# Kernel tuning notes

Measured on AMD Instinct MI355X. Metric: run time of the kernel, lower is better.

Reference implementation:

```python
import jax, jax.numpy as jnp
import numpy as np

B, T, D_IN, H, N_LAYERS, D_OUT = 256, 512, 128, 512, 3, 1


def setup_inputs() -> dict:
    key = jax.random.key(0)
    ks = jax.random.split(key, 20)
    s = 1.0 / np.sqrt(H)
    inp = {"x": jax.random.normal(ks[0], (B, T, D_IN), dtype=jnp.float32)}
    k = 1
    for l in range(N_LAYERS):
        d_in = D_IN if l == 0 else H
        inp[f"W_ih_{l}"] = jax.random.uniform(ks[k], (4 * H, d_in), minval=-s, maxval=s); k += 1
        inp[f"W_hh_{l}"] = jax.random.uniform(ks[k], (4 * H, H), minval=-s, maxval=s); k += 1
        inp[f"b_ih_{l}"] = jax.random.uniform(ks[k], (4 * H,), minval=-s, maxval=s); k += 1
        inp[f"b_hh_{l}"] = jax.random.uniform(ks[k], (4 * H,), minval=-s, maxval=s); k += 1
    inp["W_fc"] = jax.random.uniform(ks[k], (D_OUT, H), minval=-s, maxval=s); k += 1
    inp["b_fc"] = jax.random.uniform(ks[k], (D_OUT,), minval=-s, maxval=s)
    return inp


def _lstm_layer(x, W_ih, W_hh, b_ih, b_hh):
    # x: [B, T, d_in] -> hs: [B, T, H]. PyTorch gate order: i, f, g, o.
    xg = jnp.einsum("btd,gd->btg", x, W_ih) + b_ih + b_hh  # precompute input proj [B,T,4H]
    Hh = W_hh.shape[1]
    Bb = x.shape[0]

    def step(carry, xg_t):
        h, c = carry
        g = xg_t + h @ W_hh.T  # [B, 4H]
        i, f, gg, o = jnp.split(g, 4, axis=-1)
        c = jax.nn.sigmoid(f) * c + jax.nn.sigmoid(i) * jnp.tanh(gg)
        h = jax.nn.sigmoid(o) * jnp.tanh(c)
        return (h, c), h

    h0 = jnp.zeros((Bb, Hh), x.dtype)
    (_, _), hs = jax.lax.scan(step, (h0, h0), jnp.swapaxes(xg, 0, 1))
    return jnp.swapaxes(hs, 0, 1)


def reference(x, W_ih_0, W_hh_0, b_ih_0, b_hh_0,
              W_ih_1, W_hh_1, b_ih_1, b_hh_1,
              W_ih_2, W_hh_2, b_ih_2, b_hh_2,
              W_fc, b_fc):
    # Eval mode: inter-layer dropout (p=0.4) is identity.
    h = _lstm_layer(x, W_ih_0, W_hh_0, b_ih_0, b_hh_0)
    h = _lstm_layer(h, W_ih_1, W_hh_1, b_ih_1, b_hh_1)
    h = _lstm_layer(h, W_ih_2, W_hh_2, b_ih_2, b_hh_2)
    return h[:, -1, :] @ W_fc.T + b_fc  # [B, D_OUT]
```

## Files before the change

### kernel.cpp

```cpp
#include <hip/hip_runtime.h>

#define B_   256
#define T_   512
#define DIN_ 128
#define H_   512
#define G4_  2048

typedef __bf16 bf16_t;
typedef __bf16 bf16x8 __attribute__((ext_vector_type(8)));
typedef __bf16 bf16x4 __attribute__((ext_vector_type(4)));
typedef float  f32x4  __attribute__((ext_vector_type(4)));

__device__ __forceinline__ void gload16cc(const void* g, void* l) {
  __builtin_amdgcn_global_load_lds(
      (const __attribute__((address_space(1))) unsigned int*)g,
      (__attribute__((address_space(3))) unsigned int*)l, 16, 0, 17);
}

__global__ void cast_f32_bf16(const float* __restrict__ s, bf16_t* __restrict__ d, int n) {
  int i = (blockIdx.x * 256 + threadIdx.x) * 4;
  if (i >= n) return;
  float4 v = *(const float4*)(s + i);
  bf16x4 o;
  o[0] = (bf16_t)v.x; o[1] = (bf16_t)v.y; o[2] = (bf16_t)v.z; o[3] = (bf16_t)v.w;
  *(bf16x4*)(d + i) = o;
}

__global__ void cast_strided(const float* __restrict__ s, bf16_t* __restrict__ d,
                             int Ks, int Kd, int coff) {
  int npr = Ks >> 3;
  int i = blockIdx.x * 256 + threadIdx.x;
  if (i >= 2048 * npr) return;
  int row = i / npr, j = i - row * npr;
  const float* sp = s + (size_t)row * Ks + j * 8;
  float4 v0 = *(const float4*)sp;
  float4 v1 = *(const float4*)(sp + 4);
  bf16x8 o;
  o[0] = (bf16_t)v0.x; o[1] = (bf16_t)v0.y; o[2] = (bf16_t)v0.z; o[3] = (bf16_t)v0.w;
  o[4] = (bf16_t)v1.x; o[5] = (bf16_t)v1.y; o[6] = (bf16_t)v1.z; o[7] = (bf16_t)v1.w;
  *(bf16x8*)(d + (size_t)row * Kd + coff + j * 8) = o;
}

__global__ void bias_sum(const float* __restrict__ a, const float* __restrict__ b,
                         float* __restrict__ o, int n) {
  int i = blockIdx.x * 256 + threadIdx.x;
  if (i < n) o[i] = a[i] + b[i];
}

#define RING_N (8 * 256 * 512)
#define FSTR   16

template<int NKT>
__device__ __forceinline__ void step_loop(
    char* smem, const bf16_t* __restrict__ xbf, const bf16_t* __restrict__ wcl,
    const float* __restrict__ bias_l, bf16_t* ringPrev, bf16_t* ringOwn,
    float* __restrict__ hsf, int* flags, int layer, int bg, int ug)
{
  constexpr int KL   = NKT * 32;
  constexpr int ROWB = KL * 2;
  constexpr int XKT  = NKT - 16;
  constexpr bool L0  = (NKT == 20);
  const int tid  = threadIdx.x;
  const int lane = tid & 63;
  const int wv   = tid >> 6;
  const int ul   = lane & 15;
  const int grp  = lane >> 4;
  const int u0   = ug * 32;
  const int gsel = wv >> 1;
  const int usub = (wv & 1) * 16;

  bf16x8 wfrag[NKT];
  {
    const bf16_t* wrow = wcl + (size_t)(gsel * 512 + u0 + usub + ul) * KL + grp * 8;
    #pragma unroll
    for (int kk = 0; kk < NKT; ++kk) wfrag[kk] = *(const bf16x8*)(wrow + kk * 32);
  }
  const int um = tid >> 3;
  const int uq = tid & 7;
  float bsv[4][4];
  #pragma unroll
  for (int g = 0; g < 4; ++g)
    #pragma unroll
    for (int q = 0; q < 4; ++q)
      bsv[g][q] = bias_l[g * 512 + u0 + uq * 4 + q];

  float cst[4] = {0.f, 0.f, 0.f, 0.f};
  float* gatesF = (float*)smem;

  int* fl_own  = flags + ((layer * 512) * 4 + bg) * FSTR;
  int* fl_prev = flags + (((layer - 1) * 512) * 4 + bg) * FSTR;
  int* fl_next = flags + (((layer + 1) * 512) * 4 + bg) * FSTR;

  for (int s = 0; s < 512; ++s) {
    const int slot  = s & 7;
    const int slot2 = (s - 1) & 7;
    if (!L0) {
      if (tid == 0)
        while (__hip_atomic_load(fl_prev + s * 4 * FSTR, __ATOMIC_RELAXED,
                                 __HIP_MEMORY_SCOPE_AGENT) < 16)
          __builtin_amdgcn_s_sleep(1);
      __syncthreads();
      const bf16_t* prvS = ringPrev + (size_t)slot * (256 * 512) + (size_t)(bg * 64) * 512;
      #pragma unroll
      for (int i = 0; i < 8; ++i) {
        int r = i * 8 + wv;
        gload16cc(prvS + r * 512 + (lane ^ (r & 7)) * 8, smem + r * 2048);
      }
    } else {
      #pragma unroll
      for (int i2 = 0; i2 < 2; ++i2) {
        int idx = i2 * 512 + tid;
        int r = idx >> 4, cx = idx & 15;
        int px = cx ^ (r & 7);
        bf16x8 v = *(const bf16x8*)(xbf + ((size_t)(bg * 64 + r) * T_ + s) * 128 + cx * 8);
        *(bf16x8*)(smem + r * 1280 + px * 16) = v;
      }
    }
    __syncthreads();
    f32x4 acc[4] = {};
    #pragma unroll
    for (int kk = 0; kk < XKT; ++kk) {
      bf16x8 av[4];
      #pragma unroll
      for (int mt = 0; mt < 4; ++mt) {
        int r = mt * 16 + ul;
        int c = kk * 4 + grp;
        av[mt] = *(const bf16x8*)(smem + r * ROWB + (c ^ (r & 7)) * 16);
      }
      #pragma unroll
      for (int mt = 0; mt < 4; ++mt)
        acc[mt] = __builtin_amdgcn_mfma_f32_16x16x32_bf16(av[mt], wfrag[kk], acc[mt], 0, 0, 0);
    }
    if (tid == 0) {
      if (s > 0)
        while (__hip_atomic_load(fl_own + (s - 1) * 4 * FSTR, __ATOMIC_RELAXED,
                                 __HIP_MEMORY_SCOPE_AGENT) < 16)
          __builtin_amdgcn_s_sleep(1);
      if (layer < 2 && s >= 8)
        while (__hip_atomic_load(fl_next + (s - 8) * 4 * FSTR, __ATOMIC_RELAXED,
                                 __HIP_MEMORY_SCOPE_AGENT) < 16)
          __builtin_amdgcn_s_sleep(1);
    }
    __syncthreads();
    {
      const bf16_t* ownS = ringOwn + (size_t)slot2 * (256 * 512) + (size_t)(bg * 64) * 512;
      #pragma unroll
      for (int i = 0; i < 8; ++i) {
        int r = i * 8 + wv;
        const bf16_t* src = ownS + r * 512 + (lane ^ (r & 7)) * 8;
        if (L0) gload16cc(src, smem + r * 1280 + 256);
        else    gload16cc(src, smem + r * 2048 + 1024);
      }
    }
    __syncthreads();
    #pragma unroll
    for (int kk = XKT; kk < NKT; ++kk) {
      bf16x8 av[4];
      #pragma unroll
      for (int mt = 0; mt < 4; ++mt) {
        int r = mt * 16 + ul;
        int c = kk * 4 + grp;
        int pos;
        if (L0) pos = 16 + ((c - 16) ^ (r & 7));
        else    pos = c ^ (r & 7);
        av[mt] = *(const bf16x8*)(smem + r * ROWB + pos * 16);
      }
      #pragma unroll
      for (int mt = 0; mt < 4; ++mt)
        acc[mt] = __builtin_amdgcn_mfma_f32_16x16x32_bf16(av[mt], wfrag[kk], acc[mt], 0, 0, 0);
    }
    __syncthreads();
    #pragma unroll
    for (int mt = 0; mt < 4; ++mt)
      #pragma unroll
      for (int rr = 0; rr < 4; ++rr) {
        int m = mt * 16 + grp * 4 + rr;
        gatesF[m * 148 + gsel * 36 + usub + ul] = acc[mt][rr];
      }
    __syncthreads();
    f32x4 gi = *(const f32x4*)&gatesF[um * 148 +   0 + uq * 4];
    f32x4 gf = *(const f32x4*)&gatesF[um * 148 +  36 + uq * 4];
    f32x4 gg = *(const f32x4*)&gatesF[um * 148 +  72 + uq * 4];
    f32x4 go = *(const f32x4*)&gatesF[um * 148 + 108 + uq * 4];
    union { bf16x4 v; unsigned long long u; } pk;
    f32x4 hvf;
    #pragma unroll
    for (int q = 0; q < 4; ++q) {
      float i_ = gi[q] + bsv[0][q];
      float f_ = gf[q] + bsv[1][q];
      float g_ = gg[q] + bsv[2][q];
      float o_ = go[q] + bsv[3][q];
      float si = 1.f / (1.f + __expf(-i_));
      float sf = 1.f / (1.f + __expf(-f_));
      float so = 1.f / (1.f + __expf(-o_));
      float tg = 2.f / (1.f + __expf(-2.f * g_)) - 1.f;
      float cv = sf * cst[q] + si * tg;
      cst[q] = cv;
      float th = 2.f / (1.f + __expf(-2.f * cv)) - 1.f;
      hvf[q] = so * th;
      pk.v[q] = (bf16_t)hvf[q];
    }
    {
      int b = bg * 64 + um;
      bf16_t* dst = ringOwn + (size_t)slot * (256 * 512) + (size_t)b * 512 + u0 + uq * 4;
      (void)__hip_atomic_exchange((unsigned long long*)dst, pk.u,
                                  __ATOMIC_RELAXED, __HIP_MEMORY_SCOPE_AGENT);
      if (layer == 2 && s == 511)
        *(f32x4*)(hsf + (size_t)b * 512 + u0 + uq * 4) = hvf;
    }
    __syncthreads();
    if (tid == 0)
      atomicAdd(fl_own + s * 4 * FSTR, 1);
  }
}

__global__ __launch_bounds__(512, 2)
void lstm_persist(const bf16_t* __restrict__ xbf, const bf16_t* __restrict__ wc,
                  const float* __restrict__ bias, bf16_t* __restrict__ rings,
                  float* __restrict__ hsf, int* __restrict__ flags)
{
  __shared__ __align__(16) char smem[131072];
  const int bid   = blockIdx.x;
  const int layer = bid >> 6;
  const int bg    = (bid >> 4) & 3;
  const int ug    = bid & 15;
  bf16_t* ringOwn  = rings + (size_t)layer * RING_N;
  bf16_t* ringPrev = rings + (size_t)(layer - 1) * RING_N;
  if (layer == 0) {
    step_loop<20>(smem, xbf, wc, bias, ringPrev, ringOwn, hsf, flags, 0, bg, ug);
  } else {
    const bf16_t* wcl = wc + 2048 * 640 + (size_t)(layer - 1) * 2048 * 1024;
    step_loop<32>(smem, xbf, wcl, bias + layer * 2048, ringPrev, ringOwn, hsf,
                  flags, layer, bg, ug);
  }
}

__global__ void fc_kernel(const float* __restrict__ h, const float* __restrict__ Wfc,
                          const float* __restrict__ bfc, float* __restrict__ out) {
  int b = blockIdx.x;
  int l = threadIdx.x;
  const float* hp = h + (size_t)b * H_;
  float acc = 0.f;
  #pragma unroll
  for (int i = 0; i < 8; ++i) acc += hp[l + i * 64] * Wfc[l + i * 64];
  #pragma unroll
  for (int off = 32; off; off >>= 1) acc += __shfl_down(acc, off, 64);
  if (l == 0) out[b] = acc + bfc[0];
}

extern "C" void kernel_launch(void* const* d_in, const int* in_sizes, int n_in,
                              void* d_out, int out_size, void* d_ws, size_t ws_size,
                              hipStream_t stream) {
  const float* x        = (const float*)d_in[0];
  const float* Wih_f[3] = {(const float*)d_in[1], (const float*)d_in[5], (const float*)d_in[9]};
  const float* Whh_f[3] = {(const float*)d_in[2], (const float*)d_in[6], (const float*)d_in[10]};
  const float* bih_f[3] = {(const float*)d_in[3], (const float*)d_in[7], (const float*)d_in[11]};
  const float* bhh_f[3] = {(const float*)d_in[4], (const float*)d_in[8], (const float*)d_in[12]};
  const float* Wfc = (const float*)d_in[13];
  const float* bfc = (const float*)d_in[14];

  char* ws = (char*)d_ws;
  size_t off = 0;
  auto take = [&](size_t bytes) { char* p = ws + off; off = (off + bytes + 255) & ~255ULL; return p; };
  bf16_t* XBF   = (bf16_t*)take((size_t)B_ * T_ * DIN_ * 2);
  bf16_t* WC    = (bf16_t*)take((size_t)(2048*640 + 2*2048*1024) * 2);
  float*  BIAS  = (float*) take(3 * 2048 * 4);
  bf16_t* RINGS = (bf16_t*)take((size_t)3 * RING_N * 2);
  float*  HSF   = (float*) take((size_t)B_ * H_ * 4);
  int*    FLAGS = (int*)   take(3 * 512 * 4 * FSTR * 4);

  bf16_t* WC1 = WC + 2048 * 640;
  bf16_t* WC2 = WC1 + 2048 * 1024;

  cast_f32_bf16<<<16384, 256, 0, stream>>>(x, XBF, B_ * T_ * DIN_);
  cast_strided<<<128, 256, 0, stream>>>(Wih_f[0], WC,  128, 640, 0);
  cast_strided<<<512, 256, 0, stream>>>(Whh_f[0], WC,  512, 640, 128);
  cast_strided<<<512, 256, 0, stream>>>(Wih_f[1], WC1, 512, 1024, 0);
  cast_strided<<<512, 256, 0, stream>>>(Whh_f[1], WC1, 512, 1024, 512);
  cast_strided<<<512, 256, 0, stream>>>(Wih_f[2], WC2, 512, 1024, 0);
  cast_strided<<<512, 256, 0, stream>>>(Whh_f[2], WC2, 512, 1024, 512);
  for (int l = 0; l < 3; ++l)
    bias_sum<<<8, 256, 0, stream>>>(bih_f[l], bhh_f[l], BIAS + l * 2048, G4_);
  hipMemsetAsync(RINGS, 0, (size_t)3 * RING_N * 2, stream);
  hipMemsetAsync(FLAGS, 0, 3 * 512 * 4 * FSTR * 4, stream);

  lstm_persist<<<192, 512, 0, stream>>>(XBF, WC, BIAS, RINGS, HSF, FLAGS);
  fc_kernel<<<B_, 64, 0, stream>>>(HSF, Wfc, bfc, (float*)d_out);
}
```

Baseline: 3.853 ms.

## Switch recurrent step to 32x32x16 MFMA with split-K across wave halves

Replaces the 16x16x32 MFMA tiling with 32x32x16 MFMAs. Each wave now owns one gate's 32 units over 64 batch rows, and the K dimension is split between two wave groups whose partial sums are reduced through shared memory before the gate nonlinearities. The LDS swizzle is widened to 16 chunks and rows are stored at a uniform ROWB stride. The intent is fewer LDS A-fragment reads per MFMA and better matrix-core efficiency on the latency-bound per-timestep GEMM. The cost is an extra partial-sum reduction in LDS, a larger gate scratch buffer, and more accumulator registers.

```diff
diff --git a/kernel.cpp b/kernel.cpp
--- a/kernel.cpp
+++ b/kernel.cpp
@@ -10,6 +10,7 @@
 typedef __bf16 bf16x8 __attribute__((ext_vector_type(8)));
 typedef __bf16 bf16x4 __attribute__((ext_vector_type(4)));
 typedef float  f32x4  __attribute__((ext_vector_type(4)));
+typedef float  f32x16 __attribute__((ext_vector_type(16)));
 
 __device__ __forceinline__ void gload16cc(const void* g, void* l) {
   __builtin_amdgcn_global_load_lds(
@@ -50,42 +51,48 @@
 #define RING_N (8 * 256 * 512)
 #define FSTR   16
 
-template<int NKT>
+template<bool L0>
 __device__ __forceinline__ void step_loop(
     char* smem, const bf16_t* __restrict__ xbf, const bf16_t* __restrict__ wcl,
     const float* __restrict__ bias_l, bf16_t* ringPrev, bf16_t* ringOwn,
     float* __restrict__ hsf, int* flags, int layer, int bg, int ug)
 {
-  constexpr int KL   = NKT * 32;
+  constexpr int KL   = L0 ? 640 : 1024;
   constexpr int ROWB = KL * 2;
-  constexpr int XKT  = NKT - 16;
-  constexpr bool L0  = (NKT == 20);
+  constexpr int XT   = L0 ? 4 : 16;
+  constexpr int HT   = 16;
+  constexpr int NT   = XT + HT;
+  constexpr int HOFF = L0 ? 256 : 1024;
   const int tid  = threadIdx.x;
   const int lane = tid & 63;
   const int wv   = tid >> 6;
-  const int ul   = lane & 15;
-  const int grp  = lane >> 4;
+  const int g    = wv & 3;
+  const int kh   = wv >> 2;
+  const int r32  = lane & 31;
+  const int l5   = lane >> 5;
   const int u0   = ug * 32;
-  const int gsel = wv >> 1;
-  const int usub = (wv & 1) * 16;
-
-  bf16x8 wfrag[NKT];
+  const int t0x  = L0 ? (kh * 4) : (kh * 16);
+  const int t0h  = L0 ? (8 + kh * 16) : (32 + kh * 16);
+
+  bf16x8 wfrag[NT];
   {
-    const bf16_t* wrow = wcl + (size_t)(gsel * 512 + u0 + usub + ul) * KL + grp * 8;
-    #pragma unroll
-    for (int kk = 0; kk < NKT; ++kk) wfrag[kk] = *(const bf16x8*)(wrow + kk * 32);
+    const bf16_t* wrow = wcl + (size_t)(g * 512 + u0 + r32) * KL + l5 * 8;
+    #pragma unroll
+    for (int i = 0; i < XT; ++i) wfrag[i]      = *(const bf16x8*)(wrow + (t0x + i) * 16);
+    #pragma unroll
+    for (int i = 0; i < HT; ++i) wfrag[XT + i] = *(const bf16x8*)(wrow + (t0h + i) * 16);
   }
   const int um = tid >> 3;
   const int uq = tid & 7;
   float bsv[4][4];
   #pragma unroll
-  for (int g = 0; g < 4; ++g)
+  for (int g2 = 0; g2 < 4; ++g2)
     #pragma unroll
     for (int q = 0; q < 4; ++q)
-      bsv[g][q] = bias_l[g * 512 + u0 + uq * 4 + q];
+      bsv[g2][q] = bias_l[g2 * 512 + u0 + uq * 4 + q];
 
   float cst[4] = {0.f, 0.f, 0.f, 0.f};
-  float* gatesF = (float*)smem;
+  float* gp = (float*)smem;
 
   int* fl_own  = flags + ((layer * 512) * 4 + bg) * FSTR;
   int* fl_prev = flags + (((layer - 1) * 512) * 4 + bg) * FSTR;
@@ -104,32 +111,27 @@
       #pragma unroll
       for (int i = 0; i < 8; ++i) {
         int r = i * 8 + wv;
-        gload16cc(prvS + r * 512 + (lane ^ (r & 7)) * 8, smem + r * 2048);
+        gload16cc(prvS + r * 512 + (lane ^ (r & 15)) * 8, smem + r * ROWB);
       }
     } else {
       #pragma unroll
       for (int i2 = 0; i2 < 2; ++i2) {
         int idx = i2 * 512 + tid;
         int r = idx >> 4, cx = idx & 15;
-        int px = cx ^ (r & 7);
+        int px = cx ^ (r & 15);
         bf16x8 v = *(const bf16x8*)(xbf + ((size_t)(bg * 64 + r) * T_ + s) * 128 + cx * 8);
-        *(bf16x8*)(smem + r * 1280 + px * 16) = v;
-      }
-    }
-    __syncthreads();
-    f32x4 acc[4] = {};
-    #pragma unroll
-    for (int kk = 0; kk < XKT; ++kk) {
-      bf16x8 av[4];
-      #pragma unroll
-      for (int mt = 0; mt < 4; ++mt) {
-        int r = mt * 16 + ul;
-        int c = kk * 4 + grp;
-        av[mt] = *(const bf16x8*)(smem + r * ROWB + (c ^ (r & 7)) * 16);
-      }
-      #pragma unroll
-      for (int mt = 0; mt < 4; ++mt)
-        acc[mt] = __builtin_amdgcn_mfma_f32_16x16x32_bf16(av[mt], wfrag[kk], acc[mt], 0, 0, 0);
+        *(bf16x8*)(smem + r * ROWB + px * 16) = v;
+      }
+    }
+    __syncthreads();
+    f32x16 acc0 = {}, acc1 = {};
+    #pragma unroll
+    for (int i = 0; i < XT; ++i) {
+      const int px = ((t0x + i) * 2 + l5) ^ (r32 & 15);
+      bf16x8 a0 = *(const bf16x8*)(smem + r32 * ROWB + px * 16);
+      bf16x8 a1 = *(const bf16x8*)(smem + (32 + r32) * ROWB + px * 16);
+      acc0 = __builtin_amdgcn_mfma_f32_32x32x16_bf16(a0, wfrag[i], acc0, 0, 0, 0);
+      acc1 = __builtin_amdgcn_mfma_f32_32x32x16_bf16(a1, wfrag[i], acc1, 0, 0, 0);
     }
     if (tid == 0) {
       if (s > 0)
@@ -147,58 +149,56 @@
       #pragma unroll
       for (int i = 0; i < 8; ++i) {
         int r = i * 8 + wv;
-        const bf16_t* src = ownS + r * 512 + (lane ^ (r & 7)) * 8;
-        if (L0) gload16cc(src, smem + r * 1280 + 256);
-        else    gload16cc(src, smem + r * 2048 + 1024);
-      }
-    }
-    __syncthreads();
-    #pragma unroll
-    for (int kk = XKT; kk < NKT; ++kk) {
-      bf16x8 av[4];
-      #pragma unroll
-      for (int mt = 0; mt < 4; ++mt) {
-        int r = mt * 16 + ul;
-        int c = kk * 4 + grp;
-        int pos;
-        if (L0) pos = 16 + ((c - 16) ^ (r & 7));
-        else    pos = c ^ (r & 7);
-        av[mt] = *(const bf16x8*)(smem + r * ROWB + pos * 16);
-      }
-      #pragma unroll
-      for (int mt = 0; mt < 4; ++mt)
-        acc[mt] = __builtin_amdgcn_mfma_f32_16x16x32_bf16(av[mt], wfrag[kk], acc[mt], 0, 0, 0);
-    }
-    __syncthreads();
-    #pragma unroll
-    for (int mt = 0; mt < 4; ++mt)
-      #pragma unroll
-      for (int rr = 0; rr < 4; ++rr) {
-        int m = mt * 16 + grp * 4 + rr;
-        gatesF[m * 148 + gsel * 36 + usub + ul] = acc[mt][rr];
-      }
-    __syncthreads();
-    f32x4 gi = *(const f32x4*)&gatesF[um * 148 +   0 + uq * 4];
-    f32x4 gf = *(const f32x4*)&gatesF[um * 148 +  36 + uq * 4];
-    f32x4 gg = *(const f32x4*)&gatesF[um * 148 +  72 + uq * 4];
-    f32x4 go = *(const f32x4*)&gatesF[um * 148 + 108 + uq * 4];
+        gload16cc(ownS + r * 512 + (lane ^ (r & 15)) * 8, smem + r * ROWB + HOFF);
+      }
+    }
+    __syncthreads();
+    #pragma unroll
+    for (int i = 0; i < HT; ++i) {
+      const int px = ((t0h + i) * 2 + l5) ^ (r32 & 15);
+      bf16x8 a0 = *(const bf16x8*)(smem + r32 * ROWB + px * 16);
+      bf16x8 a1 = *(const bf16x8*)(smem + (32 + r32) * ROWB + px * 16);
+      acc0 = __builtin_amdgcn_mfma_f32_32x32x16_bf16(a0, wfrag[XT + i], acc0, 0, 0, 0);
+      acc1 = __builtin_amdgcn_mfma_f32_32x32x16_bf16(a1, wfrag[XT + i], acc1, 0, 0, 0);
+    }
+    __syncthreads();
+    {
+      const int base = kh * 8192 + g * 32 + r32;
+      #pragma unroll
+      for (int reg = 0; reg < 16; ++reg) {
+        int mr = (reg & 3) + 8 * (reg >> 2) + 4 * l5;
+        gp[base + mr * 128]        = acc0[reg];
+        gp[base + (32 + mr) * 128] = acc1[reg];
+      }
+    }
+    __syncthreads();
     union { bf16x4 v; unsigned long long u; } pk;
     f32x4 hvf;
-    #pragma unroll
-    for (int q = 0; q < 4; ++q) {
-      float i_ = gi[q] + bsv[0][q];
-      float f_ = gf[q] + bsv[1][q];
-      float g_ = gg[q] + bsv[2][q];
-      float o_ = go[q] + bsv[3][q];
-      float si = 1.f / (1.f + __expf(-i_));
-      float sf = 1.f / (1.f + __expf(-f_));
-      float so = 1.f / (1.f + __expf(-o_));
-      float tg = 2.f / (1.f + __expf(-2.f * g_)) - 1.f;
-      float cv = sf * cst[q] + si * tg;
-      cst[q] = cv;
-      float th = 2.f / (1.f + __expf(-2.f * cv)) - 1.f;
-      hvf[q] = so * th;
-      pk.v[q] = (bf16_t)hvf[q];
+    {
+      f32x4 gv[4];
+      #pragma unroll
+      for (int g2 = 0; g2 < 4; ++g2) {
+        f32x4 p0 = *(const f32x4*)&gp[um * 128 + g2 * 32 + uq * 4];
+        f32x4 p1 = *(const f32x4*)&gp[8192 + um * 128 + g2 * 32 + uq * 4];
+        #pragma unroll
+        for (int q = 0; q < 4; ++q) gv[g2][q] = p0[q] + p1[q];
+      }
+      #pragma unroll
+      for (int q = 0; q < 4; ++q) {
+        float i_ = gv[0][q] + bsv[0][q];
+        float f_ = gv[1][q] + bsv[1][q];
+        float g_ = gv[2][q] + bsv[2][q];
+        float o_ = gv[3][q] + bsv[3][q];
+        float si = 1.f / (1.f + __expf(-i_));
+        float sf = 1.f / (1.f + __expf(-f_));
+        float so = 1.f / (1.f + __expf(-o_));
+        float tg = 2.f / (1.f + __expf(-2.f * g_)) - 1.f;
+        float cv = sf * cst[q] + si * tg;
+        cst[q] = cv;
+        float th = 2.f / (1.f + __expf(-2.f * cv)) - 1.f;
+        hvf[q] = so * th;
+        pk.v[q] = (bf16_t)hvf[q];
+      }
     }
     {
       int b = bg * 64 + um;
@@ -227,11 +227,11 @@
   bf16_t* ringOwn  = rings + (size_t)layer * RING_N;
   bf16_t* ringPrev = rings + (size_t)(layer - 1) * RING_N;
   if (layer == 0) {
-    step_loop<20>(smem, xbf, wc, bias, ringPrev, ringOwn, hsf, flags, 0, bg, ug);
+    step_loop<true>(smem, xbf, wc, bias, ringPrev, ringOwn, hsf, flags, 0, bg, ug);
   } else {
     const bf16_t* wcl = wc + 2048 * 640 + (size_t)(layer - 1) * 2048 * 1024;
-    step_loop<32>(smem, xbf, wcl, bias + layer * 2048, ringPrev, ringOwn, hsf,
-                  flags, layer, bg, ug);
+    step_loop<false>(smem, xbf, wcl, bias + layer * 2048, ringPrev, ringOwn, hsf,
+                     flags, layer, bg, ug);
   }
 }
 
```

New measurement: 3.353 ms. 1.15x faster.
